# Kernel optimization log

Hardware: AMD Instinct MI355X
Metric: run time of the kernel (lower is better)

The kernel has to match this reference:

```python
import jax, jax.numpy as jnp
import numpy as np

D_MODEL = 768
N_HEADS = 12
D_HEAD = D_MODEL // N_HEADS


def setup_inputs() -> dict:
    key = jax.random.key(0)
    k_x, k_qw, k_qb, k_ow, k_ob = jax.random.split(key, 5)
    B, N = 2, 4096
    scale = 1.0 / np.sqrt(D_MODEL)
    return {
        "x": jax.random.normal(k_x, (B, N, D_MODEL), dtype=jnp.float32),
        # torch nn.Linear stores weight as [out_features, in_features]
        "qkv_w": jax.random.uniform(k_qw, (3 * D_MODEL, D_MODEL), jnp.float32, -scale, scale),
        "qkv_b": jax.random.uniform(k_qb, (3 * D_MODEL,), jnp.float32, -scale, scale),
        "out_w": jax.random.uniform(k_ow, (D_MODEL, D_MODEL), jnp.float32, -scale, scale),
        "out_b": jax.random.uniform(k_ob, (D_MODEL,), jnp.float32, -scale, scale),
    }


def reference(x, qkv_w, qkv_b, out_w, out_b):
    B, N, D = x.shape
    qkv = x @ qkv_w.T + qkv_b                                   # [B, N, 3D]
    qkv = qkv.reshape(B, N, 3, N_HEADS, D_HEAD)
    qkv = jnp.transpose(qkv, (2, 0, 3, 1, 4))                    # [3, B, H, N, d]
    q, k, v = qkv[0], qkv[1], qkv[2]
    scores = jnp.einsum("bhqd,bhkd->bhqk", q, k) / np.sqrt(D_HEAD)
    attn = jax.nn.softmax(scores, axis=-1)
    out = jnp.einsum("bhqk,bhkd->bhqd", attn, v)                 # [B, H, N, d]
    out = jnp.transpose(out, (0, 2, 1, 3)).reshape(B, N, D)
    return out @ out_w.T + out_b
```

## Files before the change

kernel.cpp:

```cpp
#include <hip/hip_runtime.h>
#include <cstdint>

#define SEQ 4096
#define NH 12
#define DH 64
#define DM 768
#define MT 8192
#define QKVN 2304

typedef __bf16 bf16;
typedef __attribute__((ext_vector_type(8))) __bf16 bf16x8;
typedef __attribute__((ext_vector_type(4))) __bf16 bf16x4;
typedef __attribute__((ext_vector_type(2))) __bf16 bf16x2;
typedef __attribute__((ext_vector_type(4))) float f32x4;
typedef __attribute__((ext_vector_type(16))) float f32x16;
typedef __attribute__((ext_vector_type(2))) int int2v;

__device__ __forceinline__ void async_ld16(const void* g, void* lds) {
  __builtin_amdgcn_global_load_lds(
      (__attribute__((address_space(1))) void*)(void*)g,
      (__attribute__((address_space(3))) void*)lds, 16, 0, 0);
}

__device__ __forceinline__ int sexp2_bits(float s) {
  return (int)__builtin_fmaf(s, 8388608.0f, 1065091072.0f);
}

__device__ __forceinline__ int pack_hi16(int lo, int hi) {
#if __has_builtin(__builtin_amdgcn_perm)
  return (int)__builtin_amdgcn_perm((unsigned)hi, (unsigned)lo, 0x07060302u);
#else
  return (int)(((unsigned)lo >> 16) | ((unsigned)hi & 0xffff0000u));
#endif
}

__device__ __forceinline__ void lane32_swap(int& a, int& b) {
#if __has_builtin(__builtin_amdgcn_permlane32_swap)
  int2v r = __builtin_amdgcn_permlane32_swap(a, b, false, false);
  a = r.x; b = r.y;
#else
  int hi = (threadIdx.x & 63) >> 5;
  int ra = __shfl_xor(a, 32, 64), rb = __shfl_xor(b, 32, 64);
  int na = hi ? rb : a;
  int nb = hi ? b : ra;
  a = na; b = nb;
#endif
}

#define NX4  (MT * DM / 4)
#define NW14 (QKVN * DM / 4)
#define NW24 (DM * DM / 4)
__global__ void cvt_all(const float* __restrict__ x, const float* __restrict__ w1,
                        const float* __restrict__ w2, bf16* __restrict__ xb,
                        bf16* __restrict__ wb1, bf16* __restrict__ wb2) {
  int i = blockIdx.x * blockDim.x + threadIdx.x;
  const float* src; bf16* dst; int j;
  if (i < NX4) { src = x; dst = xb; j = i; }
  else if (i < NX4 + NW14) { src = w1; dst = wb1; j = i - NX4; }
  else if (i < NX4 + NW14 + NW24) { src = w2; dst = wb2; j = i - NX4 - NW14; }
  else return;
  f32x4 v = ((const f32x4*)src)[j];
  bf16x4 o;
  o.x = (bf16)v.x; o.y = (bf16)v.y; o.z = (bf16)v.z; o.w = (bf16)v.w;
  ((bf16x4*)dst)[j] = o;
}

template<int MODE>
__global__ __launch_bounds__(256) void gemm_bt(
    const bf16* __restrict__ A, const bf16* __restrict__ Bw,
    const float* __restrict__ bias,
    bf16* __restrict__ outQ, bf16* __restrict__ outK, bf16* __restrict__ outVt,
    float* __restrict__ outF,
    int M, int N, int K)
{
  __shared__ bf16 smem[2 * 128 * 64];
  bf16* sA = smem;
  bf16* sB = smem + 128 * 64;
  bf16* sT = smem;

  const int tid  = threadIdx.x;
  const int wave = tid >> 6;
  const int lane = tid & 63;
  const int l15  = lane & 15;
  const int quad = lane >> 4;

  constexpr int NT = (MODE == 0) ? (QKVN / 128) : (DM / 128);
  const int lin = blockIdx.x;
  const int rem = lin % (NT * 8);
  const int m0 = ((lin / (NT * 8)) * 8 + (rem % 8)) * 128;
  const int n0 = (rem / 8) * 128;

  const int rowbase = (wave >> 1) * 64;
  const int colbase = (wave & 1) * 64;

  f32x4 acc[4][4] = {};

  const int srow = lane >> 3;
  const int spg  = (lane & 7) ^ srow;
  const int xk   = l15 & 7;

  for (int kt = 0; kt < K; kt += 64) {
#pragma unroll
    for (int p = 0; p < 8; ++p) {
      int chunk = p * 4 + wave;
      if (chunk < 16) {
        int row = chunk * 8 + srow;
        async_ld16(A + (size_t)(m0 + row) * K + kt + spg * 8, &sA[chunk * 512]);
      } else {
        int row = (chunk - 16) * 8 + srow;
        async_ld16(Bw + (size_t)(n0 + row) * K + kt + spg * 8, &sB[(chunk - 16) * 512]);
      }
    }
    __syncthreads();

#pragma unroll
    for (int ks = 0; ks < 2; ++ks) {
      bf16x8 af[4], bfr[4];
#pragma unroll
      for (int rt = 0; rt < 4; ++rt)
        af[rt] = *(const bf16x8*)&sA[(rowbase + rt * 16 + l15) * 64 +
                                     (((ks * 4 + quad) ^ xk) * 8)];
#pragma unroll
      for (int ct = 0; ct < 4; ++ct)
        bfr[ct] = *(const bf16x8*)&sB[(colbase + ct * 16 + l15) * 64 +
                                      (((ks * 4 + quad) ^ xk) * 8)];
#pragma unroll
      for (int rt = 0; rt < 4; ++rt)
#pragma unroll
        for (int ct = 0; ct < 4; ++ct)
          acc[rt][ct] = __builtin_amdgcn_mfma_f32_16x16x32_bf16(af[rt], bfr[ct], acc[rt][ct], 0, 0, 0);
    }
    __syncthreads();
  }

  if (MODE == 0) {
    const int g = n0 / DM;
    if (g < 2) {
      const float qscale = 0.125f * 1.4426950408889634f;
#pragma unroll
      for (int ct = 0; ct < 4; ++ct) {
        int j = n0 + colbase + ct * 16 + l15;
        float bj = bias[j];
        int f = j % DM;
        int h = f >> 6, d = f & 63;
#pragma unroll
        for (int rt = 0; rt < 4; ++rt) {
          int mrow = m0 + rowbase + rt * 16 + quad * 4;
#pragma unroll
          for (int r = 0; r < 4; ++r) {
            float v = acc[rt][ct][r] + bj;
            int m = mrow + r;
            int b = m >> 12, n = m & 4095;
            int bh = b * NH + h;
            if (g == 0) outQ[((size_t)bh * SEQ + n) * DH + d] = (bf16)(v * qscale);
            else        outK[((size_t)bh * SEQ + n) * DH + d] = (bf16)v;
          }
        }
      }
    } else {
      const int f0 = n0 - 2 * DM;
      const int b = m0 >> 12, n0m = m0 & 4095;
#pragma unroll
      for (int p = 0; p < 2; ++p) {
        __syncthreads();
        if (colbase == p * 64) {
#pragma unroll
          for (int ct = 0; ct < 4; ++ct) {
            int jl = ct * 16 + l15;
            float bj = bias[n0 + p * 64 + jl];
#pragma unroll
            for (int rt = 0; rt < 4; ++rt) {
              int ml = rowbase + rt * 16 + quad * 4;
#pragma unroll
              for (int r = 0; r < 4; ++r)
                sT[jl * 136 + ml + r] = (bf16)(acc[rt][ct][r] + bj);
            }
          }
        }
        __syncthreads();
#pragma unroll
        for (int p2 = 0; p2 < 4; ++p2) {
          int slot = p2 * 256 + tid;
          int jr = slot >> 4, mc = (slot & 15) * 8;
          int fj = f0 + p * 64 + jr;
          int h = fj >> 6, d = fj & 63;
          *(bf16x8*)&outVt[((size_t)(b * NH + h) * DH + d) * SEQ + n0m + mc] =
              *(const bf16x8*)&sT[jr * 136 + mc];
        }
      }
    }
  } else {
#pragma unroll
    for (int ct = 0; ct < 4; ++ct) {
      int j = n0 + colbase + ct * 16 + l15;
      float bj = bias[j];
#pragma unroll
      for (int rt = 0; rt < 4; ++rt) {
        int mrow = m0 + rowbase + rt * 16 + quad * 4;
#pragma unroll
        for (int r = 0; r < 4; ++r)
          outF[(size_t)(mrow + r) * N + j] = acc[rt][ct][r] + bj;
      }
    }
  }
}

__global__ __launch_bounds__(256, 3) void flash_attn(
    const bf16* __restrict__ Q, const bf16* __restrict__ Kg,
    const bf16* __restrict__ Vt, bf16* __restrict__ Oout)
{
  __shared__ bf16 sK[2][64 * 64];
  __shared__ bf16 sV[2][64 * 64];

  const int L    = blockIdx.x + (SEQ / 128) * blockIdx.y;
  const int xcd  = L & 7;
  const int slot = L >> 3;
  const int bh   = xcd + 8 * (slot >> 5);
  const int qb   = slot & 31;

  {
    int ph = (qb + bh) & 3;
    if (ph == 1) __builtin_amdgcn_s_sleep(2);
    else if (ph == 2) __builtin_amdgcn_s_sleep(4);
    else if (ph == 3) __builtin_amdgcn_s_sleep(6);
  }

  const int tid  = threadIdx.x;
  const int wave = tid >> 6;
  const int lane = tid & 63;
  const int l31  = lane & 31;
  const int hi   = lane >> 5;
  const int q0w = qb * 128 + wave * 32;

  const bf16* Qb = Q  + (size_t)bh * SEQ * DH;
  const bf16* Kb = Kg + (size_t)bh * SEQ * DH;
  const bf16* Vb = Vt + (size_t)bh * DH * SEQ;

  const int srow = lane >> 3;
  const int spg  = lane & 7;

  bf16x8 qf[4];
#pragma unroll
  for (int dc = 0; dc < 4; ++dc)
    qf[dc] = *(const bf16x8*)&Qb[(size_t)(q0w + l31) * DH + dc * 16 + hi * 8];

  f32x16 o0 = {}, o1 = {};
  float rs0 = 0.f, rs1 = 0.f, rs2 = 0.f, rs3 = 0.f;

  const int keyk = (l31 & 7) ^ (((l31 >> 3) & 3) << 1);
  int off[4];
#pragma unroll
  for (int dc = 0; dc < 4; ++dc)
    off[dc] = l31 * 64 + (((dc * 2 + hi) ^ keyk) * 8);

  auto stage = [&](int kt, int buf) {
#pragma unroll
    for (int j = 0; j < 2; ++j) {
      int r0 = wave * 16 + j * 8;
      int row = r0 + srow;
      int lg = spg ^ (row & 7) ^ (((row >> 3) & 3) << 1);
      async_ld16(Kb + (size_t)(kt + row) * DH + lg * 8, &sK[buf][r0 * 64]);
      async_ld16(Vb + (size_t)row * SEQ + kt + lg * 8, &sV[buf][r0 * 64]);
    }
  };

  auto compute = [&](const bf16* sKp, const bf16* sVp) {
#pragma unroll
    for (int kb = 0; kb < 2; ++kb) {
      f32x16 s = {};
#pragma unroll
      for (int dc = 0; dc < 4; ++dc) {
        bf16x8 kf = *(const bf16x8*)&sKp[off[dc] + kb * 2048];
        s = __builtin_amdgcn_mfma_f32_32x32x16_bf16(kf, qf[dc], s, 0, 0, 0);
      }
#pragma unroll
      for (int kc = 0; kc < 2; ++kc) {
        int b0 = sexp2_bits(s[8 * kc + 0]);
        int b1 = sexp2_bits(s[8 * kc + 1]);
        int b2 = sexp2_bits(s[8 * kc + 2]);
        int b3 = sexp2_bits(s[8 * kc + 3]);
        int b4 = sexp2_bits(s[8 * kc + 4]);
        int b5 = sexp2_bits(s[8 * kc + 5]);
        int b6 = sexp2_bits(s[8 * kc + 6]);
        int b7 = sexp2_bits(s[8 * kc + 7]);
        rs0 += __int_as_float(b0 & 0xffff0000) + __int_as_float(b4 & 0xffff0000);
        rs1 += __int_as_float(b1 & 0xffff0000) + __int_as_float(b5 & 0xffff0000);
        rs2 += __int_as_float(b2 & 0xffff0000) + __int_as_float(b6 & 0xffff0000);
        rs3 += __int_as_float(b3 & 0xffff0000) + __int_as_float(b7 & 0xffff0000);
        int g0a = pack_hi16(b0, b1);
        int g0b = pack_hi16(b2, b3);
        int g1a = pack_hi16(b4, b5);
        int g1b = pack_hi16(b6, b7);
        lane32_swap(g0a, g1a);
        lane32_swap(g0b, g1b);
        union { int i[4]; bf16x8 v; } Af;
        Af.i[0] = g0a; Af.i[1] = g0b; Af.i[2] = g1a; Af.i[3] = g1b;
        bf16x8 vf0 = *(const bf16x8*)&sVp[off[kb * 2 + kc]];
        bf16x8 vf1 = *(const bf16x8*)&sVp[off[kb * 2 + kc] + 2048];
        o0 = __builtin_amdgcn_mfma_f32_32x32x16_bf16(Af.v, vf0, o0, 0, 0, 0);
        o1 = __builtin_amdgcn_mfma_f32_32x32x16_bf16(Af.v, vf1, o1, 0, 0, 0);
      }
    }
  };

  stage(0, 0);
  __syncthreads();

  for (int kt = 0; kt < SEQ; kt += 128) {
    if (kt + 64 < SEQ) stage(kt + 64, 1);
    compute(sK[0], sV[0]);
    __syncthreads();
    if (kt + 128 < SEQ) stage(kt + 128, 0);
    compute(sK[1], sV[1]);
    __syncthreads();
  }

  float rsum = (rs0 + rs1) + (rs2 + rs3);
  rsum += __shfl_xor(rsum, 32, 64);
  float invq = 1.0f / rsum;

  const int bg = bh / NH, h = bh % NH;
#pragma unroll
  for (int i = 0; i < 16; ++i) {
    int ql = 8 * (i >> 2) + (i & 3) + 4 * hi;
    float inv = __shfl(invq, ql, 64);
    size_t base = (size_t)(bg * SEQ + q0w + ql) * DM + h * DH;
    Oout[base + l31]      = (bf16)(o0[i] * inv);
    Oout[base + 32 + l31] = (bf16)(o1[i] * inv);
  }
}

extern "C" void kernel_launch(void* const* d_in, const int* in_sizes, int n_in,
                              void* d_out, int out_size, void* d_ws, size_t ws_size,
                              hipStream_t stream) {
  const float* x     = (const float*)d_in[0];
  const float* qkv_w = (const float*)d_in[1];
  const float* qkv_b = (const float*)d_in[2];
  const float* out_w = (const float*)d_in[3];
  const float* out_b = (const float*)d_in[4];
  float* out = (float*)d_out;

  char* w = (char*)d_ws;
  bf16* xb    = (bf16*)w; w += (size_t)MT * DM * 2;
  bf16* wqkv  = (bf16*)w; w += (size_t)QKVN * DM * 2;
  bf16* wout  = (bf16*)w; w += (size_t)DM * DM * 2;
  bf16* Qw    = (bf16*)w; w += (size_t)MT * DM * 2;
  bf16* Kw    = (bf16*)w; w += (size_t)MT * DM * 2;
  bf16* Vtw   = (bf16*)w; w += (size_t)MT * DM * 2;
  bf16* attnV = (bf16*)w; w += (size_t)MT * DM * 2;

  const int tot4 = NX4 + NW14 + NW24;
  cvt_all<<<dim3((tot4 + 255) / 256), 256, 0, stream>>>(x, qkv_w, out_w, xb, wqkv, wout);

  gemm_bt<0><<<dim3((QKVN / 128) * (MT / 128)), 256, 0, stream>>>(
      xb, wqkv, qkv_b, Qw, Kw, Vtw, nullptr, MT, QKVN, DM);

  flash_attn<<<dim3(SEQ / 128, 2 * NH), 256, 0, stream>>>(Qw, Kw, Vtw, attnV);

  gemm_bt<1><<<dim3((DM / 128) * (MT / 128)), 256, 0, stream>>>(
      attnV, wout, out_b, nullptr, nullptr, nullptr, out, MT, DM, DM);
}
```

Before: 264.1 us.

## Process two 32-query tiles per wave in flash attention to reuse K/V fragments

Each wave now handles 64 queries (two 32-row Q tiles) instead of 32, so every K fragment and V fragment read from LDS feeds two MFMAs. Blocks cover 256 queries, which halves the grid and the K/V global and LDS traffic per query. The cost is doubled accumulator and score registers, which lowers the launch-bounds occupancy target from 3 to 2 blocks. With only 384 blocks, the grid may also fill the GPU less evenly.

```diff
diff --git a/kernel.cpp b/kernel.cpp
--- a/kernel.cpp
+++ b/kernel.cpp
@@ -205,18 +205,36 @@
   }
 }
 
-__global__ __launch_bounds__(256, 3) void flash_attn(
+#define SOFTPV(S, R0, R1, R2, R3, OA, OB) do {                               \
+    int b0 = sexp2_bits(S[8*kc+0]); int b1 = sexp2_bits(S[8*kc+1]);          \
+    int b2 = sexp2_bits(S[8*kc+2]); int b3 = sexp2_bits(S[8*kc+3]);          \
+    int b4 = sexp2_bits(S[8*kc+4]); int b5 = sexp2_bits(S[8*kc+5]);          \
+    int b6 = sexp2_bits(S[8*kc+6]); int b7 = sexp2_bits(S[8*kc+7]);          \
+    R0 += __int_as_float(b0 & 0xffff0000) + __int_as_float(b4 & 0xffff0000); \
+    R1 += __int_as_float(b1 & 0xffff0000) + __int_as_float(b5 & 0xffff0000); \
+    R2 += __int_as_float(b2 & 0xffff0000) + __int_as_float(b6 & 0xffff0000); \
+    R3 += __int_as_float(b3 & 0xffff0000) + __int_as_float(b7 & 0xffff0000); \
+    int g0a = pack_hi16(b0, b1), g0b = pack_hi16(b2, b3);                    \
+    int g1a = pack_hi16(b4, b5), g1b = pack_hi16(b6, b7);                    \
+    lane32_swap(g0a, g1a); lane32_swap(g0b, g1b);                            \
+    union { int i[4]; bf16x8 v; } Af_;                                       \
+    Af_.i[0] = g0a; Af_.i[1] = g0b; Af_.i[2] = g1a; Af_.i[3] = g1b;          \
+    OA = __builtin_amdgcn_mfma_f32_32x32x16_bf16(Af_.v, vf0, OA, 0, 0, 0);   \
+    OB = __builtin_amdgcn_mfma_f32_32x32x16_bf16(Af_.v, vf1, OB, 0, 0, 0);   \
+  } while (0)
+
+__global__ __launch_bounds__(256, 2) void flash_attn(
     const bf16* __restrict__ Q, const bf16* __restrict__ Kg,
     const bf16* __restrict__ Vt, bf16* __restrict__ Oout)
 {
   __shared__ bf16 sK[2][64 * 64];
   __shared__ bf16 sV[2][64 * 64];
 
-  const int L    = blockIdx.x + (SEQ / 128) * blockIdx.y;
+  const int L    = blockIdx.x + (SEQ / 256) * blockIdx.y;
   const int xcd  = L & 7;
   const int slot = L >> 3;
-  const int bh   = xcd + 8 * (slot >> 5);
-  const int qb   = slot & 31;
+  const int bh   = xcd + 8 * (slot >> 4);
+  const int qb   = slot & 15;
 
   {
     int ph = (qb + bh) & 3;
@@ -230,7 +248,7 @@
   const int lane = tid & 63;
   const int l31  = lane & 31;
   const int hi   = lane >> 5;
-  const int q0w = qb * 128 + wave * 32;
+  const int q0w  = qb * 256 + wave * 64;
 
   const bf16* Qb = Q  + (size_t)bh * SEQ * DH;
   const bf16* Kb = Kg + (size_t)bh * SEQ * DH;
@@ -239,13 +257,16 @@
   const int srow = lane >> 3;
   const int spg  = lane & 7;
 
-  bf16x8 qf[4];
-#pragma unroll
-  for (int dc = 0; dc < 4; ++dc)
-    qf[dc] = *(const bf16x8*)&Qb[(size_t)(q0w + l31) * DH + dc * 16 + hi * 8];
-
-  f32x16 o0 = {}, o1 = {};
-  float rs0 = 0.f, rs1 = 0.f, rs2 = 0.f, rs3 = 0.f;
+  bf16x8 qf0[4], qf1[4];
+#pragma unroll
+  for (int dc = 0; dc < 4; ++dc) {
+    qf0[dc] = *(const bf16x8*)&Qb[(size_t)(q0w + l31) * DH + dc * 16 + hi * 8];
+    qf1[dc] = *(const bf16x8*)&Qb[(size_t)(q0w + 32 + l31) * DH + dc * 16 + hi * 8];
+  }
+
+  f32x16 o00 = {}, o01 = {}, o10 = {}, o11 = {};
+  float r00 = 0.f, r01 = 0.f, r02 = 0.f, r03 = 0.f;
+  float r10 = 0.f, r11 = 0.f, r12 = 0.f, r13 = 0.f;
 
   const int keyk = (l31 & 7) ^ (((l31 >> 3) & 3) << 1);
   int off[4];
@@ -267,38 +288,22 @@
   auto compute = [&](const bf16* sKp, const bf16* sVp) {
 #pragma unroll
     for (int kb = 0; kb < 2; ++kb) {
-      f32x16 s = {};
+      bf16x8 kf[4];
+#pragma unroll
+      for (int dc = 0; dc < 4; ++dc)
+        kf[dc] = *(const bf16x8*)&sKp[off[dc] + kb * 2048];
+      f32x16 s0 = {}, s1 = {};
 #pragma unroll
       for (int dc = 0; dc < 4; ++dc) {
-        bf16x8 kf = *(const bf16x8*)&sKp[off[dc] + kb * 2048];
-        s = __builtin_amdgcn_mfma_f32_32x32x16_bf16(kf, qf[dc], s, 0, 0, 0);
+        s0 = __builtin_amdgcn_mfma_f32_32x32x16_bf16(kf[dc], qf0[dc], s0, 0, 0, 0);
+        s1 = __builtin_amdgcn_mfma_f32_32x32x16_bf16(kf[dc], qf1[dc], s1, 0, 0, 0);
       }
 #pragma unroll
       for (int kc = 0; kc < 2; ++kc) {
-        int b0 = sexp2_bits(s[8 * kc + 0]);
-        int b1 = sexp2_bits(s[8 * kc + 1]);
-        int b2 = sexp2_bits(s[8 * kc + 2]);
-        int b3 = sexp2_bits(s[8 * kc + 3]);
-        int b4 = sexp2_bits(s[8 * kc + 4]);
-        int b5 = sexp2_bits(s[8 * kc + 5]);
-        int b6 = sexp2_bits(s[8 * kc + 6]);
-        int b7 = sexp2_bits(s[8 * kc + 7]);
-        rs0 += __int_as_float(b0 & 0xffff0000) + __int_as_float(b4 & 0xffff0000);
-        rs1 += __int_as_float(b1 & 0xffff0000) + __int_as_float(b5 & 0xffff0000);
-        rs2 += __int_as_float(b2 & 0xffff0000) + __int_as_float(b6 & 0xffff0000);
-        rs3 += __int_as_float(b3 & 0xffff0000) + __int_as_float(b7 & 0xffff0000);
-        int g0a = pack_hi16(b0, b1);
-        int g0b = pack_hi16(b2, b3);
-        int g1a = pack_hi16(b4, b5);
-        int g1b = pack_hi16(b6, b7);
-        lane32_swap(g0a, g1a);
-        lane32_swap(g0b, g1b);
-        union { int i[4]; bf16x8 v; } Af;
-        Af.i[0] = g0a; Af.i[1] = g0b; Af.i[2] = g1a; Af.i[3] = g1b;
         bf16x8 vf0 = *(const bf16x8*)&sVp[off[kb * 2 + kc]];
         bf16x8 vf1 = *(const bf16x8*)&sVp[off[kb * 2 + kc] + 2048];
-        o0 = __builtin_amdgcn_mfma_f32_32x32x16_bf16(Af.v, vf0, o0, 0, 0, 0);
-        o1 = __builtin_amdgcn_mfma_f32_32x32x16_bf16(Af.v, vf1, o1, 0, 0, 0);
+        SOFTPV(s0, r00, r01, r02, r03, o00, o01);
+        SOFTPV(s1, r10, r11, r12, r13, o10, o11);
       }
     }
   };
@@ -315,18 +320,25 @@
     __syncthreads();
   }
 
-  float rsum = (rs0 + rs1) + (rs2 + rs3);
-  rsum += __shfl_xor(rsum, 32, 64);
-  float invq = 1.0f / rsum;
+  float rsum0 = (r00 + r01) + (r02 + r03);
+  rsum0 += __shfl_xor(rsum0, 32, 64);
+  float inv0 = 1.0f / rsum0;
+  float rsum1 = (r10 + r11) + (r12 + r13);
+  rsum1 += __shfl_xor(rsum1, 32, 64);
+  float inv1 = 1.0f / rsum1;
 
   const int bg = bh / NH, h = bh % NH;
 #pragma unroll
   for (int i = 0; i < 16; ++i) {
     int ql = 8 * (i >> 2) + (i & 3) + 4 * hi;
-    float inv = __shfl(invq, ql, 64);
-    size_t base = (size_t)(bg * SEQ + q0w + ql) * DM + h * DH;
-    Oout[base + l31]      = (bf16)(o0[i] * inv);
-    Oout[base + 32 + l31] = (bf16)(o1[i] * inv);
+    float iva = __shfl(inv0, ql, 64);
+    size_t basea = (size_t)(bg * SEQ + q0w + ql) * DM + h * DH;
+    Oout[basea + l31]      = (bf16)(o00[i] * iva);
+    Oout[basea + 32 + l31] = (bf16)(o01[i] * iva);
+    float ivb = __shfl(inv1, ql, 64);
+    size_t baseb = (size_t)(bg * SEQ + q0w + 32 + ql) * DM + h * DH;
+    Oout[baseb + l31]      = (bf16)(o10[i] * ivb);
+    Oout[baseb + 32 + l31] = (bf16)(o11[i] * ivb);
   }
 }
 
@@ -355,7 +367,7 @@
   gemm_bt<0><<<dim3((QKVN / 128) * (MT / 128)), 256, 0, stream>>>(
       xb, wqkv, qkv_b, Qw, Kw, Vtw, nullptr, MT, QKVN, DM);
 
-  flash_attn<<<dim3(SEQ / 128, 2 * NH), 256, 0, stream>>>(Qw, Kw, Vtw, attnV);
+  flash_attn<<<dim3(SEQ / 256, 2 * NH), 256, 0, stream>>>(Qw, Kw, Vtw, attnV);
 
   gemm_bt<1><<<dim3((DM / 128) * (MT / 128)), 256, 0, stream>>>(
       attnV, wout, out_b, nullptr, nullptr, nullptr, out, MT, DM, DM);
```

Result: slower. 283.8 us (+7.5%).

## Double-buffer GEMM K-loop, remap block order, stage Q/K epilogue through LDS

Applied to the files above, without the earlier changes.

The GEMM main loop now uses two LDS buffers, so the async global-to-LDS loads for the next K tile are issued before the MFMA work on the current tile, with one barrier per iteration instead of two. Block indices are permuted with a stride-8 interleave to change which tiles run concurrently, which may affect L2 reuse. The Q/K epilogue now writes bias-added, scaled tiles into shared memory and then stores 16-byte vectors per row, replacing scattered 2-byte global stores. LDS use doubles to 64 KB per block, which may reduce occupancy.

```diff
diff --git a/kernel.cpp b/kernel.cpp
--- a/kernel.cpp
+++ b/kernel.cpp
@@ -7,6 +7,7 @@
 #define DM 768
 #define MT 8192
 #define QKVN 2304
+#define BH 24
 
 typedef __bf16 bf16;
 typedef __attribute__((ext_vector_type(8))) __bf16 bf16x8;
@@ -73,9 +74,7 @@
     float* __restrict__ outF,
     int M, int N, int K)
 {
-  __shared__ bf16 smem[2 * 128 * 64];
-  bf16* sA = smem;
-  bf16* sB = smem + 128 * 64;
+  __shared__ bf16 smem[2 * 2 * 128 * 64];
   bf16* sT = smem;
 
   const int tid  = threadIdx.x;
@@ -85,9 +84,11 @@
   const int quad = lane >> 4;
 
   constexpr int NT = (MODE == 0) ? (QKVN / 128) : (DM / 128);
+  constexpr int CPX = NT * 8;
   const int lin = blockIdx.x;
-  const int rem = lin % (NT * 8);
-  const int m0 = ((lin / (NT * 8)) * 8 + (rem % 8)) * 128;
+  const int v   = (lin & 7) * CPX + (lin >> 3);
+  const int rem = v % CPX;
+  const int m0 = ((v / CPX) * 8 + (rem % 8)) * 128;
   const int n0 = (rem / 8) * 128;
 
   const int rowbase = (wave >> 1) * 64;
@@ -99,7 +100,9 @@
   const int spg  = (lane & 7) ^ srow;
   const int xk   = l15 & 7;
 
-  for (int kt = 0; kt < K; kt += 64) {
+  auto stageg = [&](int kt, int buf) {
+    bf16* sA = smem + buf * 16384;
+    bf16* sB = sA + 8192;
 #pragma unroll
     for (int p = 0; p < 8; ++p) {
       int chunk = p * 4 + wave;
@@ -111,8 +114,11 @@
         async_ld16(Bw + (size_t)(n0 + row) * K + kt + spg * 8, &sB[(chunk - 16) * 512]);
       }
     }
-    __syncthreads();
-
+  };
+
+  auto computeg = [&](int buf) {
+    const bf16* sA = smem + buf * 16384;
+    const bf16* sB = sA + 8192;
 #pragma unroll
     for (int ks = 0; ks < 2; ++ks) {
       bf16x8 af[4], bfr[4];
@@ -130,31 +136,52 @@
         for (int ct = 0; ct < 4; ++ct)
           acc[rt][ct] = __builtin_amdgcn_mfma_f32_16x16x32_bf16(af[rt], bfr[ct], acc[rt][ct], 0, 0, 0);
     }
+  };
+
+  stageg(0, 0);
+  __syncthreads();
+  int buf = 0;
+  for (int kt = 64; kt < K; kt += 64) {
+    stageg(kt, buf ^ 1);
+    computeg(buf);
     __syncthreads();
-  }
+    buf ^= 1;
+  }
+  computeg(buf);
 
   if (MODE == 0) {
     const int g = n0 / DM;
     if (g < 2) {
-      const float qscale = 0.125f * 1.4426950408889634f;
-#pragma unroll
-      for (int ct = 0; ct < 4; ++ct) {
-        int j = n0 + colbase + ct * 16 + l15;
-        float bj = bias[j];
-        int f = j % DM;
-        int h = f >> 6, d = f & 63;
-#pragma unroll
-        for (int rt = 0; rt < 4; ++rt) {
-          int mrow = m0 + rowbase + rt * 16 + quad * 4;
-#pragma unroll
-          for (int r = 0; r < 4; ++r) {
-            float v = acc[rt][ct][r] + bj;
-            int m = mrow + r;
-            int b = m >> 12, n = m & 4095;
-            int bh = b * NH + h;
-            if (g == 0) outQ[((size_t)bh * SEQ + n) * DH + d] = (bf16)(v * qscale);
-            else        outK[((size_t)bh * SEQ + n) * DH + d] = (bf16)v;
+      const float sc = (g == 0) ? 0.125f * 1.4426950408889634f : 1.0f;
+      bf16* outQK = (g == 0) ? outQ : outK;
+      const int f0q = n0 - g * DM;
+      const int b = m0 >> 12, n0m = m0 & 4095;
+#pragma unroll
+      for (int p = 0; p < 2; ++p) {
+        __syncthreads();
+        if (colbase == p * 64) {
+#pragma unroll
+          for (int ct = 0; ct < 4; ++ct) {
+            int c = ct * 16 + l15;
+            float bj = bias[n0 + p * 64 + c];
+#pragma unroll
+            for (int rt = 0; rt < 4; ++rt) {
+              int ml = rowbase + rt * 16 + quad * 4;
+#pragma unroll
+              for (int r = 0; r < 4; ++r)
+                sT[(ml + r) * 72 + c] = (bf16)((acc[rt][ct][r] + bj) * sc);
+            }
           }
+        }
+        __syncthreads();
+        const int h = (f0q + p * 64) >> 6;
+        const int bh = b * NH + h;
+#pragma unroll
+        for (int p2 = 0; p2 < 4; ++p2) {
+          int slot = p2 * 256 + tid;
+          int mr = slot >> 3, cg = slot & 7;
+          *(bf16x8*)&outQK[((size_t)bh * SEQ + n0m + mr) * DH + cg * 8] =
+              *(const bf16x8*)&sT[mr * 72 + cg * 8];
         }
       }
     } else {
```

Result: faster. 257.5 us (-2.5%).
